# Performance work log

Hardware: AMD Instinct MI355X
Metric: run time of the kernel (lower is better)

## Reference

```python
import jax, jax.numpy as jnp
import numpy as np

B, S, C, H = 2, 2048, 1280, 20
D = C // H  # head_dim = 64


def setup_inputs() -> dict:
    key = jax.random.key(0)
    ks = jax.random.split(key, 5)
    scale = 1.0 / np.sqrt(C)
    return {
        "hidden_states": jax.random.normal(ks[0], (B, S, C), dtype=jnp.float32),
        "Wq": jax.random.normal(ks[1], (C, C), dtype=jnp.float32) * scale,
        "Wk": jax.random.normal(ks[2], (C, C), dtype=jnp.float32) * scale,
        "Wv": jax.random.normal(ks[3], (C, C), dtype=jnp.float32) * scale,
        "Wo": jax.random.normal(ks[4], (C, C), dtype=jnp.float32) * scale,
        "bo": jnp.zeros((C,), dtype=jnp.float32),
    }


def reference(hidden_states, Wq, Wk, Wv, Wo, bo):
    residual = hidden_states
    # q/k/v projections (self-attention: encoder_hidden_states is None)
    q = hidden_states @ Wq  # [B,S,C]
    k = hidden_states @ Wk
    v = hidden_states @ Wv
    # split heads -> [B,H,S,D]
    q = q.reshape(B, S, H, D).transpose(0, 2, 1, 3)
    k = k.reshape(B, S, H, D).transpose(0, 2, 1, 3)
    v = v.reshape(B, S, H, D).transpose(0, 2, 1, 3)
    scale = 1.0 / np.sqrt(D)
    scores = jnp.einsum('bhqd,bhkd->bhqk', q, k) * scale  # [B,H,S,S]
    attn_probs = jax.nn.softmax(scores, axis=-1)
    # loss term: Frobenius norm of the full attention-prob tensor (fp32)
    loss = jnp.sqrt(jnp.sum(jnp.square(attn_probs.astype(jnp.float32))))
    out = jnp.einsum('bhqk,bhkd->bhqd', attn_probs, v)  # [B,H,S,D]
    out = out.transpose(0, 2, 1, 3).reshape(B, S, C)
    out = out @ Wo + bo
    out = out + residual  # residual_connection=True, rescale_output_factor=1.0
    return out, loss
```

## Files before the change

kernel.cpp:

```cpp
#include <hip/hip_runtime.h>
#include <hip/hip_bf16.h>
#include <math.h>

#define B_SZ   2
#define S_LEN  2048
#define C_DIM  1280
#define H_NUM  20
#define D_HEAD 64
#define M_TOT  (B_SZ * S_LEN)

typedef __bf16 bf16;
typedef __bf16 bf16x8 __attribute__((ext_vector_type(8)));
typedef __bf16 bf16x4 __attribute__((ext_vector_type(4)));
typedef float  f32x4  __attribute__((ext_vector_type(4)));

__device__ inline f32x4 zero4() { f32x4 z; z[0]=z[1]=z[2]=z[3]=0.f; return z; }

__device__ __forceinline__ void async_copy16(void* lds, const void* g) {
    __builtin_amdgcn_global_load_lds(
        (const __attribute__((address_space(1))) unsigned int*)g,
        (__attribute__((address_space(3))) unsigned int*)lds,
        16, 0, 0);
}

__global__ __launch_bounds__(256) void k_convert_hs(const float* __restrict__ in,
                                                    bf16* __restrict__ out) {
    int i = (blockIdx.x * 256 + threadIdx.x) * 4;
    float4 v = *(const float4*)(in + i);
    bf16x4 o; o[0]=(bf16)v.x; o[1]=(bf16)v.y; o[2]=(bf16)v.z; o[3]=(bf16)v.w;
    *(bf16x4*)(out + i) = o;
}

__global__ __launch_bounds__(256) void k_transpose_w(
    const float* __restrict__ w0, const float* __restrict__ w1,
    const float* __restrict__ w2, const float* __restrict__ w3,
    bf16* __restrict__ o0, bf16* __restrict__ o1,
    bf16* __restrict__ o2, bf16* __restrict__ o3) {
    __shared__ float t[32][33];
    const float* w = blockIdx.z==0 ? w0 : blockIdx.z==1 ? w1 : blockIdx.z==2 ? w2 : w3;
    bf16*       o  = blockIdx.z==0 ? o0 : blockIdx.z==1 ? o1 : blockIdx.z==2 ? o2 : o3;
    int k0 = blockIdx.y*32, n0 = blockIdx.x*32;
    int tx = threadIdx.x & 31, ty = threadIdx.x >> 5;
    #pragma unroll
    for (int i = 0; i < 32; i += 8)
        t[ty+i][tx] = w[(size_t)(k0+ty+i)*C_DIM + n0 + tx];
    __syncthreads();
    #pragma unroll
    for (int i = 0; i < 32; i += 8)
        o[(size_t)(n0+ty+i)*C_DIM + k0 + tx] = (bf16)t[tx][ty+i];
}

#define QBM 256
#define QBN 256
#define QBK 32
#define QNT (C_DIM / QBK)
__global__ __launch_bounds__(512, 2) void k_gemm_qkv(
    const bf16* __restrict__ A,
    const bf16* __restrict__ Wcat,
    bf16* __restrict__ Qo, bf16* __restrict__ Ko, bf16* __restrict__ VTo) {
    __shared__ bf16 lds[3][2][QBM][QBK];
    const int m0  = blockIdx.y * QBM;
    const int nx  = blockIdx.x;
    const int z   = nx / 5;
    const int nw0 = (nx % 5) * QBN;
    const int ng0 = nx * QBN;
    const int tid = threadIdx.x, lane = tid & 63, wid = tid >> 6;
    const int wm = wid >> 2, wn = wid & 3;
    const int g = lane >> 4, lr = lane & 15;
    const float scale = (z==0) ? 0.18033688011112042f : 1.0f;

    f32x4 acc[8][4];
    #pragma unroll
    for (int i=0;i<8;i++)
        #pragma unroll
        for (int j=0;j<4;j++)
            acc[i][j] = zero4();

#define QSTAGE(bf, kt)                                                       \
    { const int k0_ = (kt)*QBK;                                              \
      _Pragma("unroll")                                                      \
      for (int c = 0; c < 2; ++c) {                                          \
        int p = c*512 + tid;                                                 \
        int row = p >> 2, gp = p & 3;                                        \
        async_copy16((char*)&lds[bf][0][0][0] + p*16,                        \
                     &A[(size_t)(m0+row)*C_DIM + k0_ + gp*8]);               \
        async_copy16((char*)&lds[bf][1][0][0] + p*16,                        \
                     &Wcat[(size_t)(ng0+row)*C_DIM + k0_ + gp*8]);           \
      } }

    QSTAGE(0, 0);
    QSTAGE(1, 1);
    asm volatile("s_waitcnt vmcnt(4)" ::: "memory");
    __builtin_amdgcn_s_barrier();

    int cur = 0;
    for (int t = 0; t < QNT; ++t) {
        if (t + 2 < QNT) {
            int sb = cur + 2; if (sb >= 3) sb -= 3;
            QSTAGE(sb, t + 2);
        }
        const bf16* AB = &lds[cur][0][0][0];
        const bf16* BB = &lds[cur][1][0][0];
        bf16x8 af[8], bfr[4];
        #pragma unroll
        for (int mf = 0; mf < 8; ++mf)
            af[mf] = *(const bf16x8*)(AB + (wm*128 + mf*16 + lr)*QBK + g*8);
        #pragma unroll
        for (int nf = 0; nf < 4; ++nf)
            bfr[nf] = *(const bf16x8*)(BB + (wn*64 + nf*16 + lr)*QBK + g*8);
        #pragma unroll
        for (int mf = 0; mf < 8; ++mf)
            #pragma unroll
            for (int nf = 0; nf < 4; ++nf)
                acc[mf][nf] = __builtin_amdgcn_mfma_f32_16x16x32_bf16(
                    af[mf], bfr[nf], acc[mf][nf], 0,0,0);
        if (t + 2 < QNT) asm volatile("s_waitcnt vmcnt(4) lgkmcnt(0)" ::: "memory");
        else             asm volatile("s_waitcnt vmcnt(0) lgkmcnt(0)" ::: "memory");
        __builtin_amdgcn_s_barrier();
        if (++cur == 3) cur = 0;
    }

    if (z == 2) {
        #pragma unroll
        for (int mf=0;mf<8;mf++) {
            #pragma unroll
            for (int nf=0;nf<4;nf++) {
                int n = nw0 + wn*64 + nf*16 + lr;
                int h = n >> 6, d = n & 63;
                int m = m0 + wm*128 + mf*16 + g*4;
                int b = m >> 11, s = m & (S_LEN-1);
                bf16x4 ov;
                #pragma unroll
                for (int r=0;r<4;r++) ov[r] = (bf16)acc[mf][nf][r];
                *(bf16x4*)&VTo[((size_t)(b*H_NUM + h)*D_HEAD + d)*S_LEN + s] = ov;
            }
        }
    } else {
        bf16* Out = (z==0) ? Qo : Ko;
        #pragma unroll
        for (int mf=0;mf<8;mf++) {
            #pragma unroll
            for (int nf=0;nf<4;nf++) {
                int n = nw0 + wn*64 + nf*16 + lr;
                int h = n >> 6, d = n & 63;
                #pragma unroll
                for (int r=0;r<4;r++) {
                    int m = m0 + wm*128 + mf*16 + g*4 + r;
                    int b = m >> 11, s = m & (S_LEN-1);
                    Out[(size_t)((b*H_NUM + h)*S_LEN + s)*D_HEAD + d] = (bf16)(acc[mf][nf][r] * scale);
                }
            }
        }
    }
}

#define BM 128
#define BN 128
#define BK 64

#define GEMM_STAGE(Al, Bl, Aptr, Bptr, m0, n0, k0)                                \
    {                                                                             \
        _Pragma("unroll")                                                         \
        for (int c = 0; c < 4; ++c) {                                             \
            int p = c*256 + tid;                                                  \
            int row = p >> 3, gp = p & 7, gc = gp ^ (row & 7);                    \
            async_copy16((char*)(Al) + p*16,                                      \
                         &Aptr[(size_t)((m0)+row)*C_DIM + (k0) + gc*8]);          \
            async_copy16((char*)(Bl) + p*16,                                      \
                         &Bptr[(size_t)((n0)+row)*C_DIM + (k0) + gc*8]);          \
        }                                                                         \
    }

#define GEMM_COMPUTE(Al, Bl)                                                      \
    {                                                                             \
        _Pragma("unroll")                                                         \
        for (int kk = 0; kk < 2; ++kk) {                                          \
            bf16x8 af[4], bfr[4];                                                 \
            _Pragma("unroll")                                                     \
            for (int mf = 0; mf < 4; ++mf) {                                      \
                int arow = wm*64 + mf*16 + lr;                                    \
                af[mf] = *(const bf16x8*)((char*)(Al) + arow*128 +                \
                          (((kk*4 + g) ^ (arow & 7)) << 4));                      \
            }                                                                     \
            _Pragma("unroll")                                                     \
            for (int nf = 0; nf < 4; ++nf) {                                      \
                int brow = wn*64 + nf*16 + lr;                                    \
                bfr[nf] = *(const bf16x8*)((char*)(Bl) + brow*128 +               \
                          (((kk*4 + g) ^ (brow & 7)) << 4));                      \
            }                                                                     \
            _Pragma("unroll")                                                     \
            for (int mf = 0; mf < 4; ++mf)                                        \
                _Pragma("unroll")                                                 \
                for (int nf = 0; nf < 4; ++nf)                                    \
                    acc[mf][nf] = __builtin_amdgcn_mfma_f32_16x16x32_bf16(        \
                        af[mf], bfr[nf], acc[mf][nf], 0,0,0);                     \
        }                                                                         \
    }

__global__ __launch_bounds__(256) void k_gemm_out(
    const bf16* __restrict__ A,
    const bf16* __restrict__ WoT,
    const float* __restrict__ bo,
    const float* __restrict__ res,
    float* __restrict__ out) {
    __shared__ bf16 Al[2][BM][BK];
    __shared__ bf16 Bl[2][BN][BK];
    const int m0 = blockIdx.y * BM, n0 = blockIdx.x * BN;
    const int tid = threadIdx.x, lane = tid & 63, wid = tid >> 6;
    const int wm = wid >> 1, wn = wid & 1;
    const int g = lane >> 4, lr = lane & 15;
    f32x4 acc[4][4];
    #pragma unroll
    for (int i=0;i<4;i++)
        #pragma unroll
        for (int j=0;j<4;j++)
            acc[i][j] = zero4();
    GEMM_STAGE(&Al[0][0][0], &Bl[0][0][0], A, WoT, m0, n0, 0);
    asm volatile("s_waitcnt vmcnt(0)" ::: "memory");
    __builtin_amdgcn_s_barrier();
    int cur = 0;
    for (int k0 = 0; k0 < C_DIM; k0 += BK) {
        if (k0 + BK < C_DIM)
            GEMM_STAGE(&Al[cur^1][0][0], &Bl[cur^1][0][0], A, WoT, m0, n0, k0 + BK);
        GEMM_COMPUTE(&Al[cur][0][0], &Bl[cur][0][0]);
        asm volatile("s_waitcnt vmcnt(0) lgkmcnt(0)" ::: "memory");
        __builtin_amdgcn_s_barrier();
        cur ^= 1;
    }
    #pragma unroll
    for (int mf=0;mf<4;mf++) {
        #pragma unroll
        for (int nf=0;nf<4;nf++) {
            int n = n0 + wn*64 + nf*16 + lr;
            float bias = bo[n];
            #pragma unroll
            for (int r=0;r<4;r++) {
                int m = m0 + wm*64 + mf*16 + g*4 + r;
                size_t idx = (size_t)m*C_DIM + n;
                out[idx] = acc[mf][nf][r] + bias + res[idx];
            }
        }
    }
}

#define KVB 64
__global__ __launch_bounds__(256) void k_attn(
    const bf16* __restrict__ Q,
    const bf16* __restrict__ Kg,
    const bf16* __restrict__ VT,
    bf16* __restrict__ O,
    float* __restrict__ lossPart) {
    __shared__ bf16 Kl[2][KVB][64];
    __shared__ bf16 Vl[2][D_HEAD][64];

    const int id  = blockIdx.x;
    const int fid = (id & 7) * 80 + (id >> 3);
    const int bh = fid >> 4;
    const int qb = fid & 15;
    const int b = bh / H_NUM, hh = bh % H_NUM;
    const int tid = threadIdx.x, lane = tid & 63, wid = tid >> 6;
    const int g = lane >> 4, lr = lane & 15;

    const bf16* Kbase = Kg + (size_t)bh * S_LEN * D_HEAD;
    const bf16* Vbase = VT + (size_t)bh * D_HEAD * S_LEN;

    bf16x8 aq[2][2];
    int qrow[2];
    #pragma unroll
    for (int h=0; h<2; ++h) {
        qrow[h] = qb*128 + h*64 + wid*16 + lr;
        const bf16* qp = Q + ((size_t)bh*S_LEN + qrow[h])*D_HEAD;
        aq[h][0] = *(const bf16x8*)(qp + g*8);
        aq[h][1] = *(const bf16x8*)(qp + 32 + g*8);
    }

    bf16x8 ones;
    #pragma unroll
    for (int i=0;i<8;i++) ones[i] = (bf16)1.0f;

    const int lb7 = (lr & 3) | (((lr >> 2) & 1) << 2);
    const int lhi = ((lr >> 2) & 2) << 3;

    f32x4 o_acc[2][4];
    f32x4 l_acc[2], s2m[2];
    #pragma unroll
    for (int h=0;h<2;++h) {
        #pragma unroll
        for (int i=0;i<4;i++) o_acc[h][i] = zero4();
        l_acc[h] = zero4(); s2m[h] = zero4();
    }

#define STAGE(buf, kv0)                                                          \
    {                                                                            \
        _Pragma("unroll")                                                        \
        for (int pp=0; pp<2; ++pp) {                                             \
            int p = pp*256 + tid;                                                \
            int lrow = p >> 3, gp = p & 7;                                       \
            int tl = (lrow & 51) | ((lrow & 4) << 1) | ((lrow & 8) >> 1);        \
            async_copy16((char*)&Kl[buf][0][0] + p*16,                           \
                         Kbase + (size_t)((kv0) + tl)*D_HEAD                     \
                               + ((gp ^ (lrow & 7)) << 3));                      \
        }                                                                        \
        _Pragma("unroll")                                                        \
        for (int pp=0; pp<2; ++pp) {                                             \
            int p = pp*256 + tid;                                                \
            int drow = p >> 3, gp = p & 7;                                       \
            async_copy16((char*)&Vl[buf][0][0] + p*16,                           \
                         Vbase + (size_t)drow*S_LEN + (kv0)                      \
                               + ((gp ^ (drow & 7)) << 3));                      \
        }                                                                        \
    }

    STAGE(0, 0);
    __syncthreads();

    for (int t = 0; t < S_LEN/KVB; ++t) {
        const int cur = t & 1;
        if (t + 1 < S_LEN/KVB) STAGE(cur^1, (t+1)*KVB);
        const bf16* KB = &Kl[cur][0][0];
        const bf16* VB = &Vl[cur][0][0];

        f32x4 accp[2][2][2];
        __builtin_amdgcn_s_setprio(1);
        #pragma unroll
        for (int pair=0; pair<2; ++pair)
            #pragma unroll
            for (int u=0; u<2; ++u) {
                const bf16* kr = KB + (pair*32 + (u<<3) + lhi + lb7)*64;
                bf16x8 k0 = *(const bf16x8*)(kr + ((g       ^ lb7) << 3));
                bf16x8 k1 = *(const bf16x8*)(kr + (((4 + g) ^ lb7) << 3));
                #pragma unroll
                for (int h=0; h<2; ++h) {
                    f32x4 c = zero4();
                    c = __builtin_amdgcn_mfma_f32_16x16x32_bf16(k0, aq[h][0], c, 0,0,0);
                    c = __builtin_amdgcn_mfma_f32_16x16x32_bf16(k1, aq[h][1], c, 0,0,0);
                    accp[h][pair][u] = c;
                }
            }
        __builtin_amdgcn_s_setprio(0);
        bf16x8 pb[2][2];
        #pragma unroll
        for (int h=0; h<2; ++h)
            #pragma unroll
            for (int pair=0; pair<2; ++pair)
                #pragma unroll
                for (int u=0; u<2; ++u)
                    #pragma unroll
                    for (int r=0; r<4; ++r) {
                        float e = __builtin_amdgcn_exp2f(accp[h][pair][u][r]);
                        pb[h][pair][u*4+r] = (bf16)e;
                    }
        __builtin_amdgcn_s_setprio(1);
        #pragma unroll
        for (int h=0; h<2; ++h) {
            l_acc[h] = __builtin_amdgcn_mfma_f32_16x16x32_bf16(ones, pb[h][0], l_acc[h], 0,0,0);
            l_acc[h] = __builtin_amdgcn_mfma_f32_16x16x32_bf16(ones, pb[h][1], l_acc[h], 0,0,0);
            s2m[h]   = __builtin_amdgcn_mfma_f32_16x16x32_bf16(pb[h][0], pb[h][0], s2m[h], 0,0,0);
            s2m[h]   = __builtin_amdgcn_mfma_f32_16x16x32_bf16(pb[h][1], pb[h][1], s2m[h], 0,0,0);
        }
        #pragma unroll
        for (int ds_=0; ds_<4; ++ds_) {
            const bf16* vr = VB + (ds_*16 + lr)*64;
            #pragma unroll
            for (int pair=0; pair<2; ++pair) {
                bf16x8 v = *(const bf16x8*)(vr + (((pair*4 + g) ^ (lr & 7)) << 3));
                #pragma unroll
                for (int h=0; h<2; ++h)
                    o_acc[h][ds_] = __builtin_amdgcn_mfma_f32_16x16x32_bf16(v, pb[h][pair], o_acc[h][ds_], 0,0,0);
            }
        }
        __builtin_amdgcn_s_setprio(0);
        __syncthreads();
    }

    float lfull[2];
    #pragma unroll
    for (int h=0; h<2; ++h) {
        lfull[h] = l_acc[h][0];
        const float inv = 1.0f / lfull[h];
        bf16* orow = O + ((size_t)(b*S_LEN + qrow[h])*H_NUM + hh)*D_HEAD;
        #pragma unroll
        for (int ds_=0; ds_<4; ++ds_) {
            bf16x4 ov;
            #pragma unroll
            for (int r=0; r<4; ++r) ov[r] = (bf16)(o_acc[h][ds_][r] * inv);
            *(bf16x4*)(orow + ds_*16 + g*4) = ov;
        }
    }
    float v = 0.f;
    if (g == (lr >> 2)) {
        v  = s2m[0][lr & 3] / (lfull[0] * lfull[0]);
        v += s2m[1][lr & 3] / (lfull[1] * lfull[1]);
    }
    #pragma unroll
    for (int msk=1; msk<64; msk<<=1) v += __shfl_xor(v, msk);
    if (lane == 0) lossPart[(bh*16 + qb)*4 + wid] = v;
}

__global__ __launch_bounds__(256) void k_loss(const float* __restrict__ part,
                                              float* __restrict__ out, int n) {
    __shared__ float w[4];
    float s = 0.f;
    for (int i = threadIdx.x; i < n; i += 256) s += part[i];
    #pragma unroll
    for (int msk=1; msk<64; msk<<=1) s += __shfl_xor(s, msk);
    int lane = threadIdx.x & 63, wid = threadIdx.x >> 6;
    if (lane==0) w[wid] = s;
    __syncthreads();
    if (threadIdx.x==0) out[(size_t)M_TOT*C_DIM] = sqrtf(w[0]+w[1]+w[2]+w[3]);
}

extern "C" void kernel_launch(void* const* d_in, const int* in_sizes, int n_in,
                              void* d_out, int out_size, void* d_ws, size_t ws_size,
                              hipStream_t stream) {
    (void)in_sizes; (void)n_in; (void)out_size; (void)ws_size;
    const float* hs = (const float*)d_in[0];
    const float* Wq = (const float*)d_in[1];
    const float* Wk = (const float*)d_in[2];
    const float* Wv = (const float*)d_in[3];
    const float* Wo = (const float*)d_in[4];
    const float* bo = (const float*)d_in[5];
    float* out = (float*)d_out;

    constexpr size_t HS_E = (size_t)M_TOT * C_DIM;
    constexpr size_t W_E  = (size_t)C_DIM * C_DIM;
    char* ws = (char*)d_ws;
    size_t off = 0;
    bf16* hs_bf = (bf16*)(ws + off); off += HS_E * 2;
    bf16* WqT   = (bf16*)(ws + off); off += W_E * 2;
    bf16* WkT   = (bf16*)(ws + off); off += W_E * 2;
    bf16* WvT   = (bf16*)(ws + off); off += W_E * 2;
    bf16* WoT   = (bf16*)(ws + off); off += W_E * 2;
    bf16* Qb    = (bf16*)(ws + off); off += HS_E * 2;
    bf16* Kb    = (bf16*)(ws + off); off += HS_E * 2;
    bf16* Vtb   = (bf16*)(ws + off); off += HS_E * 2;
    bf16* Ob    = (bf16*)(ws + off); off += HS_E * 2;
    float* lossPart = (float*)(ws + off); off += 2560 * 4;

    k_convert_hs<<<HS_E/(256*4), 256, 0, stream>>>(hs, hs_bf);
    k_transpose_w<<<dim3(C_DIM/32, C_DIM/32, 4), 256, 0, stream>>>(Wq, Wk, Wv, Wo, WqT, WkT, WvT, WoT);
    k_gemm_qkv<<<dim3(3*C_DIM/QBN, M_TOT/QBM), 512, 0, stream>>>(hs_bf, WqT, Qb, Kb, Vtb);
    k_attn<<<640, 256, 0, stream>>>(Qb, Kb, Vtb, Ob, lossPart);
    k_gemm_out<<<dim3(C_DIM/BN, M_TOT/BM), 256, 0, stream>>>(Ob, WoT, bo, hs, out);
    k_loss<<<1, 256, 0, stream>>>(lossPart, out, 2560);
}
```

Before: 181.5 us.

## Merge prep kernels, fold loss reduction into out GEMM, triple-buffer 512-thread attention

Combines the hidden-state conversion and weight transpose into a single launch, and moves the final loss reduction into the output GEMM's first block, removing two kernel launches. The attention kernel now runs 512 threads per block, each covering 256 query rows. This halves the grid to 320 blocks and doubles K/V tile reuse per load. It also adds a three-stage LDS ring with partial vmcnt waits so loads run two tiles ahead. Costs include fewer blocks than before on a large CU count and more LDS per block.

```diff
diff --git a/kernel.cpp b/kernel.cpp
--- a/kernel.cpp
+++ b/kernel.cpp
@@ -23,23 +23,26 @@
         16, 0, 0);
 }
 
-__global__ __launch_bounds__(256) void k_convert_hs(const float* __restrict__ in,
-                                                    bf16* __restrict__ out) {
-    int i = (blockIdx.x * 256 + threadIdx.x) * 4;
-    float4 v = *(const float4*)(in + i);
-    bf16x4 o; o[0]=(bf16)v.x; o[1]=(bf16)v.y; o[2]=(bf16)v.z; o[3]=(bf16)v.w;
-    *(bf16x4*)(out + i) = o;
-}
-
-__global__ __launch_bounds__(256) void k_transpose_w(
+__global__ __launch_bounds__(256) void k_prep(
+    const float* __restrict__ hs, bf16* __restrict__ hs_bf,
     const float* __restrict__ w0, const float* __restrict__ w1,
     const float* __restrict__ w2, const float* __restrict__ w3,
     bf16* __restrict__ o0, bf16* __restrict__ o1,
     bf16* __restrict__ o2, bf16* __restrict__ o3) {
+    if (blockIdx.x < 5120) {
+        int i = (blockIdx.x * 256 + threadIdx.x) * 4;
+        float4 v = *(const float4*)(hs + i);
+        bf16x4 o; o[0]=(bf16)v.x; o[1]=(bf16)v.y; o[2]=(bf16)v.z; o[3]=(bf16)v.w;
+        *(bf16x4*)(hs_bf + i) = o;
+        return;
+    }
     __shared__ float t[32][33];
-    const float* w = blockIdx.z==0 ? w0 : blockIdx.z==1 ? w1 : blockIdx.z==2 ? w2 : w3;
-    bf16*       o  = blockIdx.z==0 ? o0 : blockIdx.z==1 ? o1 : blockIdx.z==2 ? o2 : o3;
-    int k0 = blockIdx.y*32, n0 = blockIdx.x*32;
+    int idx = blockIdx.x - 5120;
+    int zi  = idx / 1600;
+    int rem = idx % 1600;
+    int k0 = (rem / 40) * 32, n0 = (rem % 40) * 32;
+    const float* w = zi==0 ? w0 : zi==1 ? w1 : zi==2 ? w2 : w3;
+    bf16*       o  = zi==0 ? o0 : zi==1 ? o1 : zi==2 ? o2 : o3;
     int tx = threadIdx.x & 31, ty = threadIdx.x >> 5;
     #pragma unroll
     for (int i = 0; i < 32; i += 8)
@@ -202,9 +205,11 @@
     const bf16* __restrict__ WoT,
     const float* __restrict__ bo,
     const float* __restrict__ res,
-    float* __restrict__ out) {
+    float* __restrict__ out,
+    const float* __restrict__ lossPart, int nLoss) {
     __shared__ bf16 Al[2][BM][BK];
     __shared__ bf16 Bl[2][BN][BK];
+    __shared__ float wred[4];
     const int m0 = blockIdx.y * BM, n0 = blockIdx.x * BN;
     const int tid = threadIdx.x, lane = tid & 63, wid = tid >> 6;
     const int wm = wid >> 1, wn = wid & 1;
@@ -241,22 +246,32 @@
             }
         }
     }
+    if (blockIdx.x == 0 && blockIdx.y == 0) {
+        float s = 0.f;
+        for (int i = tid; i < nLoss; i += 256) s += lossPart[i];
+        #pragma unroll
+        for (int msk=1; msk<64; msk<<=1) s += __shfl_xor(s, msk);
+        if (lane == 0) wred[wid] = s;
+        __syncthreads();
+        if (tid == 0) out[(size_t)M_TOT*C_DIM] = sqrtf(wred[0]+wred[1]+wred[2]+wred[3]);
+    }
 }
 
 #define KVB 64
-__global__ __launch_bounds__(256) void k_attn(
+#define NT_ (S_LEN / KVB)
+__global__ __launch_bounds__(512) void k_attn(
     const bf16* __restrict__ Q,
     const bf16* __restrict__ Kg,
     const bf16* __restrict__ VT,
     bf16* __restrict__ O,
     float* __restrict__ lossPart) {
-    __shared__ bf16 Kl[2][KVB][64];
-    __shared__ bf16 Vl[2][D_HEAD][64];
+    __shared__ bf16 Kl[3][KVB][64];
+    __shared__ bf16 Vl[3][D_HEAD][64];
 
     const int id  = blockIdx.x;
-    const int fid = (id & 7) * 80 + (id >> 3);
-    const int bh = fid >> 4;
-    const int qb = fid & 15;
+    const int fid = (id & 7) * 40 + (id >> 3);
+    const int bh = fid >> 3;
+    const int qb = fid & 7;
     const int b = bh / H_NUM, hh = bh % H_NUM;
     const int tid = threadIdx.x, lane = tid & 63, wid = tid >> 6;
     const int g = lane >> 4, lr = lane & 15;
@@ -268,7 +283,7 @@
     int qrow[2];
     #pragma unroll
     for (int h=0; h<2; ++h) {
-        qrow[h] = qb*128 + h*64 + wid*16 + lr;
+        qrow[h] = qb*256 + wid*32 + h*16 + lr;
         const bf16* qp = Q + ((size_t)bh*S_LEN + qrow[h])*D_HEAD;
         aq[h][0] = *(const bf16x8*)(qp + g*8);
         aq[h][1] = *(const bf16x8*)(qp + 32 + g*8);
@@ -292,18 +307,16 @@
 
 #define STAGE(buf, kv0)                                                          \
     {                                                                            \
-        _Pragma("unroll")                                                        \
-        for (int pp=0; pp<2; ++pp) {                                             \
-            int p = pp*256 + tid;                                                \
+        {                                                                        \
+            int p = tid;                                                         \
             int lrow = p >> 3, gp = p & 7;                                       \
             int tl = (lrow & 51) | ((lrow & 4) << 1) | ((lrow & 8) >> 1);        \
             async_copy16((char*)&Kl[buf][0][0] + p*16,                           \
                          Kbase + (size_t)((kv0) + tl)*D_HEAD                     \
                                + ((gp ^ (lrow & 7)) << 3));                      \
         }                                                                        \
-        _Pragma("unroll")                                                        \
-        for (int pp=0; pp<2; ++pp) {                                             \
-            int p = pp*256 + tid;                                                \
+        {                                                                        \
+            int p = tid;                                                         \
             int drow = p >> 3, gp = p & 7;                                       \
             async_copy16((char*)&Vl[buf][0][0] + p*16,                           \
                          Vbase + (size_t)drow*S_LEN + (kv0)                      \
@@ -312,11 +325,16 @@
     }
 
     STAGE(0, 0);
-    __syncthreads();
-
-    for (int t = 0; t < S_LEN/KVB; ++t) {
-        const int cur = t & 1;
-        if (t + 1 < S_LEN/KVB) STAGE(cur^1, (t+1)*KVB);
+    STAGE(1, KVB);
+    asm volatile("s_waitcnt vmcnt(2)" ::: "memory");
+    __builtin_amdgcn_s_barrier();
+
+    int cur = 0;
+    for (int t = 0; t < NT_; ++t) {
+        if (t + 2 < NT_) {
+            int sb = cur + 2; if (sb >= 3) sb -= 3;
+            STAGE(sb, (t+2)*KVB);
+        }
         const bf16* KB = &Kl[cur][0][0];
         const bf16* VB = &Vl[cur][0][0];
 
@@ -370,7 +388,10 @@
             }
         }
         __builtin_amdgcn_s_setprio(0);
-        __syncthreads();
+        if (t + 2 < NT_) asm volatile("s_waitcnt vmcnt(2) lgkmcnt(0)" ::: "memory");
+        else             asm volatile("s_waitcnt vmcnt(0) lgkmcnt(0)" ::: "memory");
+        __builtin_amdgcn_s_barrier();
+        if (++cur == 3) cur = 0;
     }
 
     float lfull[2];
@@ -394,20 +415,7 @@
     }
     #pragma unroll
     for (int msk=1; msk<64; msk<<=1) v += __shfl_xor(v, msk);
-    if (lane == 0) lossPart[(bh*16 + qb)*4 + wid] = v;
-}
-
-__global__ __launch_bounds__(256) void k_loss(const float* __restrict__ part,
-                                              float* __restrict__ out, int n) {
-    __shared__ float w[4];
-    float s = 0.f;
-    for (int i = threadIdx.x; i < n; i += 256) s += part[i];
-    #pragma unroll
-    for (int msk=1; msk<64; msk<<=1) s += __shfl_xor(s, msk);
-    int lane = threadIdx.x & 63, wid = threadIdx.x >> 6;
-    if (lane==0) w[wid] = s;
-    __syncthreads();
-    if (threadIdx.x==0) out[(size_t)M_TOT*C_DIM] = sqrtf(w[0]+w[1]+w[2]+w[3]);
+    if (lane == 0) lossPart[(bh*8 + qb)*8 + wid] = v;
 }
 
 extern "C" void kernel_launch(void* const* d_in, const int* in_sizes, int n_in,
@@ -437,10 +445,8 @@
     bf16* Ob    = (bf16*)(ws + off); off += HS_E * 2;
     float* lossPart = (float*)(ws + off); off += 2560 * 4;
 
-    k_convert_hs<<<HS_E/(256*4), 256, 0, stream>>>(hs, hs_bf);
-    k_transpose_w<<<dim3(C_DIM/32, C_DIM/32, 4), 256, 0, stream>>>(Wq, Wk, Wv, Wo, WqT, WkT, WvT, WoT);
+    k_prep<<<11520, 256, 0, stream>>>(hs, hs_bf, Wq, Wk, Wv, Wo, WqT, WkT, WvT, WoT);
     k_gemm_qkv<<<dim3(3*C_DIM/QBN, M_TOT/QBM), 512, 0, stream>>>(hs_bf, WqT, Qb, Kb, Vtb);
-    k_attn<<<640, 256, 0, stream>>>(Qb, Kb, Vtb, Ob, lossPart);
-    k_gemm_out<<<dim3(C_DIM/BN, M_TOT/BM), 256, 0, stream>>>(Ob, WoT, bo, hs, out);
-    k_loss<<<1, 256, 0, stream>>>(lossPart, out, 2560);
-}
+    k_attn<<<320, 512, 0, stream>>>(Qb, Kb, Vtb, Ob, lossPart);
+    k_gemm_out<<<dim3(C_DIM/BN, M_TOT/BM), 256, 0, stream>>>(Ob, WoT, bo, hs, out, lossPart, 2560);
+}
```

Measured after the change: 155.3 us. 1.17x faster.
